# Performance work log

Measured on AMD Instinct MI355X. Metric: run time of the kernel, lower is better.

Reference implementation:

```python
import jax, jax.numpy as jnp
import numpy as np

EMBED_DIM = 1024
NUM_HEADS = 8
PROJ_DIM = EMBED_DIM // NUM_HEADS  # 128
SIGMA = 1.0        # attn_param
DISP = 1           # attn_displacement
BATCH = 8
SEQ_LEN = 2048
# per-head hard-coded attention positions (length == num_heads)
POSITIONS = ['center', 'left', 'right', 'first', 'last', 'center', 'left', 'right']


def _head_centers(L):
    """Center of the analytic Gaussian per head and per query position. [H, L]"""
    i = jnp.arange(L, dtype=jnp.float32)
    centers = []
    for pos in POSITIONS:
        if pos == 'center':
            c = i
        elif pos == 'left':
            c = i - DISP
        elif pos == 'right':
            c = i + DISP
        elif pos == 'first':
            c = jnp.zeros_like(i)
        else:  # 'last' (no padding: last valid index is L-1)
            c = jnp.full_like(i, L - 1)
        centers.append(c)
    return jnp.stack(centers)  # [H, L]


def setup_inputs() -> dict:
    key = jax.random.key(0)
    k1, k2, k3 = jax.random.split(key, 3)
    x = jax.random.normal(k1, (BATCH, SEQ_LEN, EMBED_DIM), dtype=jnp.float32)
    # xavier-ish scale for square weights
    s = (6.0 / (EMBED_DIM + EMBED_DIM)) ** 0.5
    W_in = jax.random.uniform(k2, (EMBED_DIM, EMBED_DIM), dtype=jnp.float32, minval=-s, maxval=s)
    W_out = jax.random.uniform(k3, (EMBED_DIM, EMBED_DIM), dtype=jnp.float32, minval=-s, maxval=s)
    return {"x": x, "W_in": W_in, "W_out": W_out}


def reference(x, W_in, W_out):
    B, L, E = x.shape
    H, P = NUM_HEADS, PROJ_DIM
    # value projection (F.linear with input_weights), split into heads
    v = (x @ W_in.T).reshape(B, L, H, P).transpose(0, 2, 1, 3)  # [B, H, L, P]
    # analytic per-head attention weights: Gaussian in key-position around center
    j = jnp.arange(L, dtype=jnp.float32)
    c = _head_centers(L)                                         # [H, Lq]
    logits = -((j[None, None, :] - c[:, :, None]) ** 2) / (2.0 * SIGMA ** 2)  # [H, Lq, Lk]
    w = jax.nn.softmax(logits, axis=-1)                          # [H, Lq, Lk]
    # weighted value aggregation (torch.bmm(attn_weights, values) per head)
    attended = jnp.einsum('hqk,bhkp->bhqp', w, v)                # [B, H, L, P]
    attended = attended.transpose(0, 2, 1, 3).reshape(B, L, E)
    # bias-free output projection
    return attended @ W_out.T
```

## Files before the change

### kernel.cpp

```cpp
#include <hip/hip_runtime.h>
#include <stdint.h>

typedef unsigned short u16;
typedef unsigned int   u32;

typedef float  f32x4  __attribute__((ext_vector_type(4)));
typedef __bf16 bf16x8 __attribute__((ext_vector_type(8)));

__device__ __forceinline__ u16 f2bf(float f) {
  union { float f; u32 u; } c; c.f = f;
  u32 u = c.u + 0x7fffu + ((c.u >> 16) & 1u);
  return (u16)(u >> 16);
}
__device__ __forceinline__ float bf2f(u16 h) {
  union { u32 u; float f; } c; c.u = ((u32)h) << 16;
  return c.f;
}
__device__ __forceinline__ void gll16(const void* g, void* l) {
  __builtin_amdgcn_global_load_lds(
      (const __attribute__((address_space(1))) void*)g,
      (__attribute__((address_space(3))) void*)l, 16, 0, 0);
}

__global__ __launch_bounds__(256)
void cvt_all(const float4* __restrict__ x,  uint2* __restrict__ xb,  int n4x,
             const float4* __restrict__ wi, uint2* __restrict__ wib,
             const float4* __restrict__ wo, uint2* __restrict__ wob, int n4w) {
  int i = blockIdx.x * 256 + threadIdx.x;
  const float4* s; uint2* d; int j;
  if (i < n4x)            { s = x;  d = xb;  j = i; }
  else if (i < n4x + n4w) { s = wi; d = wib; j = i - n4x; }
  else                    { s = wo; d = wob; j = i - n4x - n4w; }
  float4 v = s[j];
  uint2 o;
  o.x = (u32)f2bf(v.x) | ((u32)f2bf(v.y) << 16);
  o.y = (u32)f2bf(v.z) | ((u32)f2bf(v.w) << 16);
  d[j] = o;
}

template <bool OUT_BF16>
__global__ __launch_bounds__(512, 2)
void gemm_nt_256(const u16* __restrict__ A, const u16* __restrict__ B,
                 void* __restrict__ Cout, int M, int N, int K) {
  __shared__ u16 Ls[65536];
  const int tid  = threadIdx.x;
  const int lane = tid & 63;
  const int wave = tid >> 6;
  const int wm   = wave >> 2;
  const int wn   = wave & 3;
  const int ml   = lane & 15;
  const int q    = lane >> 4;
  const int qx   = q ^ (ml & 3);
  const int hx   = (ml >> 2) & 1;

  const int flat = blockIdx.y * 4 + blockIdx.x;
  const int xcd  = flat & 7;
  const int slot = flat >> 3;
  const int mt   = xcd * (gridDim.y >> 3) + (slot >> 2);
  const int nt   = slot & 3;
  const int m0   = mt * 256;
  const int n0   = nt * 256;

  const int srr = tid >> 3;
  const int gc  = (tid & 7) ^ ((tid >> 3) & 7);
  const u16* Agb = A + (size_t)(m0 + srr) * K + gc * 8;
  const u16* Bgb = B + (size_t)(n0 + srr) * K + gc * 8;
  char* LsB = (char*)Ls;
  const int wlds = wave * 1024;

  auto stageA = [&](int bufb, int h, int k0) {
    char* d = LsB + bufb + h * 16384 + wlds;
    gll16(Agb + (size_t)(h * 128) * K + k0, d);
    gll16(Agb + (size_t)(h * 128 + 64) * K + k0, d + 8192);
  };
  auto stageB = [&](int bufb, int h, int k0) {
    char* d = LsB + bufb + 32768 + h * 16384 + wlds;
    gll16(Bgb + (size_t)(h * 128) * K + k0, d);
    gll16(Bgb + (size_t)(h * 128 + 64) * K + k0, d + 8192);
  };

  const int aB_ = wm * 8192 + ml * 64 + qx * 8;
  const int bB_ = 16384 + (wn >> 1) * 8192 + ((wn & 1) * 64 + ml) * 64 + qx * 8;

  f32x4  acc[8][4] = {};
  bf16x8 fa0[4], fa1[4], B0[4], B1[4];

  auto rdA = [&](bf16x8* dst, int bw, int MH, int s) {
    const int so = (s ^ hx) * 32;
#pragma unroll
    for (int i = 0; i < 4; ++i)
      dst[i] = *reinterpret_cast<const bf16x8*>(&Ls[bw + aB_ + MH * 4096 + i * 1024 + so]);
  };
  auto rdB = [&](bf16x8* dst, int bw, int s) {
    const int so = (s ^ hx) * 32;
#pragma unroll
    for (int j = 0; j < 4; ++j)
      dst[j] = *reinterpret_cast<const bf16x8*>(&Ls[bw + bB_ + j * 1024 + so]);
  };
  auto mfma16 = [&](int mh, const bf16x8* a, const bf16x8* b) {
    __builtin_amdgcn_s_setprio(1);
#pragma unroll
    for (int i = 0; i < 4; ++i)
#pragma unroll
      for (int j = 0; j < 4; ++j)
        acc[mh * 4 + i][j] = __builtin_amdgcn_mfma_f32_16x16x32_bf16(
            a[i], b[j], acc[mh * 4 + i][j], 0, 0, 0);
    __builtin_amdgcn_s_setprio(0);
  };
  auto barrier = [&] {
    __builtin_amdgcn_sched_barrier(0);
    __builtin_amdgcn_s_barrier();
  };

  stageB(0, 0, 0);      stageB(0, 1, 0);
  stageA(0, 0, 0);      stageA(0, 1, 0);
  stageB(65536, 0, 64); stageB(65536, 1, 64);
  stageA(65536, 0, 64); stageA(65536, 1, 64);
  asm volatile("s_waitcnt vmcnt(8)" ::: "memory");
  barrier();
  rdA(fa0, 0, 0, 0);
  rdB(B0, 0, 0);

  const int NT = K >> 6;
  int bufb = 0;
  for (int t = 0; t < NT; ++t, bufb ^= 65536) {
    const int  bw     = bufb >> 1;
    const int  bwn    = (bufb ^ 65536) >> 1;
    const bool rdnext = (t + 1 < NT);
    const bool stg    = (t + 2 < NT);
    const int  kst    = (t + 2) << 6;
    mfma16(0, fa0, B0);
    rdA(fa1, bw, 0, 1); rdB(B1, bw, 1);
    barrier();
    mfma16(0, fa1, B1);
    rdA(fa0, bw, 1, 0);
    if (stg) { stageB(bufb, 0, kst); stageB(bufb, 1, kst); }
    barrier();
    mfma16(1, fa0, B0);
    rdA(fa1, bw, 1, 1);
    if (stg)         { asm volatile("s_waitcnt vmcnt(4)" ::: "memory"); }
    else if (rdnext) { asm volatile("s_waitcnt vmcnt(0)" ::: "memory"); }
    barrier();
    mfma16(1, fa1, B1);
    if (rdnext) { rdA(fa0, bwn, 0, 0); rdB(B0, bwn, 0); }
    if (stg) { stageA(bufb, 0, kst); stageA(bufb, 1, kst); }
    barrier();
  }

  const int rowb = m0 + wm * 128 + q * 4;
  const int colb = n0 + wn * 64 + ml;
#pragma unroll
  for (int mf = 0; mf < 8; ++mf)
#pragma unroll
    for (int nf = 0; nf < 4; ++nf)
#pragma unroll
      for (int r = 0; r < 4; ++r) {
        size_t idx = (size_t)(rowb + mf * 16 + r) * N + (colb + nf * 16);
        float val = acc[mf][nf][r];
        if (OUT_BF16) ((u16*)Cout)[idx] = f2bf(val);
        else          ((float*)Cout)[idx] = val;
      }
}

__global__ __launch_bounds__(256)
void gauss_conv(const u16* __restrict__ v, u16* __restrict__ att, int L) {
  constexpr float wt[13] = {
    1.5229979744712628e-08f, 3.7266531720786709e-06f, 3.3546262790251185e-04f,
    1.1108996538242306e-02f, 1.3533528323661270e-01f, 6.0653065971263342e-01f,
    1.0f,
    6.0653065971263342e-01f, 1.3533528323661270e-01f, 1.1108996538242306e-02f,
    3.3546262790251185e-04f, 3.7266531720786709e-06f, 1.5229979744712628e-08f
  };
  const int t  = threadIdx.x;
  const int fg = t & 15;
  const int li = t >> 4;
  const int l  = blockIdx.x * 16 + li;
  const int h  = blockIdx.y;
  const int b  = blockIdx.z;
  int c;
  switch (h) {
    case 0: case 5: c = l;     break;
    case 1: case 6: c = l - 1; break;
    case 2: case 7: c = l + 1; break;
    case 3:         c = 0;     break;
    default:        c = L - 1; break;
  }
  const int fbase = h * 128 + fg * 8;
  const u16* vb = v + (size_t)b * L * 1024 + fbase;

  float a[8] = {};
  float Z = 0.f;
#pragma unroll
  for (int d = -6; d <= 6; ++d) {
    int idx = c + d;
    bool ok = (idx >= 0) && (idx < L);
    int ic_ = idx < 0 ? 0 : (idx >= L ? L - 1 : idx);
    float w = ok ? wt[d + 6] : 0.f;
    Z += w;
    uint4 p = *reinterpret_cast<const uint4*>(vb + (size_t)ic_ * 1024);
    a[0] = fmaf(w, bf2f((u16)(p.x & 0xffffu)), a[0]);
    a[1] = fmaf(w, bf2f((u16)(p.x >> 16)),     a[1]);
    a[2] = fmaf(w, bf2f((u16)(p.y & 0xffffu)), a[2]);
    a[3] = fmaf(w, bf2f((u16)(p.y >> 16)),     a[3]);
    a[4] = fmaf(w, bf2f((u16)(p.z & 0xffffu)), a[4]);
    a[5] = fmaf(w, bf2f((u16)(p.z >> 16)),     a[5]);
    a[6] = fmaf(w, bf2f((u16)(p.w & 0xffffu)), a[6]);
    a[7] = fmaf(w, bf2f((u16)(p.w >> 16)),     a[7]);
  }
  float inv = 1.0f / Z;
  uint4 o;
  o.x = (u32)f2bf(a[0] * inv) | ((u32)f2bf(a[1] * inv) << 16);
  o.y = (u32)f2bf(a[2] * inv) | ((u32)f2bf(a[3] * inv) << 16);
  o.z = (u32)f2bf(a[4] * inv) | ((u32)f2bf(a[5] * inv) << 16);
  o.w = (u32)f2bf(a[6] * inv) | ((u32)f2bf(a[7] * inv) << 16);
  *reinterpret_cast<uint4*>(att + (size_t)(b * L + l) * 1024 + fbase) = o;
}

extern "C" void kernel_launch(void* const* d_in, const int* in_sizes, int n_in,
                              void* d_out, int out_size, void* d_ws, size_t ws_size,
                              hipStream_t stream) {
  const int Bb = 8, L = 2048, E = 1024;
  const int M = Bb * L, N = E, K = E;

  const float* x  = (const float*)d_in[0];
  const float* Wi = (const float*)d_in[1];
  const float* Wo = (const float*)d_in[2];
  float* out = (float*)d_out;

  size_t offV  = (size_t)M * E * 2;
  size_t offWi = offV + (size_t)M * E * 2;
  size_t offWo = offWi + (size_t)E * E * 2;
  size_t need  = offWo + (size_t)E * E * 2;
  if (ws_size < need) return;

  u16* xb  = (u16*)d_ws;
  u16* v   = (u16*)((char*)d_ws + offV);
  u16* wib = (u16*)((char*)d_ws + offWi);
  u16* wob = (u16*)((char*)d_ws + offWo);
  u16* att = xb;

  int n4x = M * E / 4, n4w = E * E / 4;
  int nblk = (n4x + 2 * n4w) / 256;
  cvt_all<<<nblk, 256, 0, stream>>>((const float4*)x, (uint2*)xb, n4x,
                                    (const float4*)Wi, (uint2*)wib,
                                    (const float4*)Wo, (uint2*)wob, n4w);

  dim3 gg(N / 256, M / 256);
  gemm_nt_256<true ><<<gg, 512, 0, stream>>>(xb,  wib, v,   M, N, K);
  gauss_conv<<<dim3(L / 16, 8, Bb), 256, 0, stream>>>(v, att, L);
  gemm_nt_256<false><<<gg, 512, 0, stream>>>(att, wob, out, M, N, K);
}
```

Measured before the change: 210.5 us.

## Restructure GEMM main loop into quadrant-based single-prefetch schedule

Result: no change. 213.7 us (+1.5%).

```diff
diff --git a/kernel.cpp b/kernel.cpp
--- a/kernel.cpp
+++ b/kernel.cpp
@@ -68,83 +68,84 @@
   char* LsB = (char*)Ls;
   const int wlds = wave * 1024;
 
-  auto stageA = [&](int bufb, int h, int k0) {
-    char* d = LsB + bufb + h * 16384 + wlds;
-    gll16(Agb + (size_t)(h * 128) * K + k0, d);
-    gll16(Agb + (size_t)(h * 128 + 64) * K + k0, d + 8192);
-  };
-  auto stageB = [&](int bufb, int h, int k0) {
-    char* d = LsB + bufb + 32768 + h * 16384 + wlds;
-    gll16(Bgb + (size_t)(h * 128) * K + k0, d);
-    gll16(Bgb + (size_t)(h * 128 + 64) * K + k0, d + 8192);
+  auto stageAll = [&](int bufb, int k0) {
+#pragma unroll
+    for (int h = 0; h < 2; ++h) {
+      char* d = LsB + bufb + h * 16384 + wlds;
+      gll16(Agb + (size_t)(h * 128) * K + k0, d);
+      gll16(Agb + (size_t)(h * 128 + 64) * K + k0, d + 8192);
+    }
+#pragma unroll
+    for (int h = 0; h < 2; ++h) {
+      char* d = LsB + bufb + 32768 + h * 16384 + wlds;
+      gll16(Bgb + (size_t)(h * 128) * K + k0, d);
+      gll16(Bgb + (size_t)(h * 128 + 64) * K + k0, d + 8192);
+    }
   };
 
   const int aB_ = wm * 8192 + ml * 64 + qx * 8;
   const int bB_ = 16384 + (wn >> 1) * 8192 + ((wn & 1) * 64 + ml) * 64 + qx * 8;
 
   f32x4  acc[8][4] = {};
-  bf16x8 fa0[4], fa1[4], B0[4], B1[4];
-
-  auto rdA = [&](bf16x8* dst, int bw, int MH, int s) {
-    const int so = (s ^ hx) * 32;
+  bf16x8 af[4][2];
+  bf16x8 bq[2][2][2];
+
+  auto rdA = [&](int bw, int mh) {
 #pragma unroll
     for (int i = 0; i < 4; ++i)
-      dst[i] = *reinterpret_cast<const bf16x8*>(&Ls[bw + aB_ + MH * 4096 + i * 1024 + so]);
-  };
-  auto rdB = [&](bf16x8* dst, int bw, int s) {
-    const int so = (s ^ hx) * 32;
-#pragma unroll
-    for (int j = 0; j < 4; ++j)
-      dst[j] = *reinterpret_cast<const bf16x8*>(&Ls[bw + bB_ + j * 1024 + so]);
-  };
-  auto mfma16 = [&](int mh, const bf16x8* a, const bf16x8* b) {
+#pragma unroll
+      for (int s = 0; s < 2; ++s)
+        af[i][s] = *reinterpret_cast<const bf16x8*>(
+            &Ls[bw + aB_ + mh * 4096 + i * 1024 + (s ^ hx) * 32]);
+  };
+  auto rdB = [&](int bw, int nh) {
+#pragma unroll
+    for (int j = 0; j < 2; ++j)
+#pragma unroll
+      for (int s = 0; s < 2; ++s)
+        bq[nh][j][s] = *reinterpret_cast<const bf16x8*>(
+            &Ls[bw + bB_ + nh * 2048 + j * 1024 + (s ^ hx) * 32]);
+  };
+  auto mfmaQ = [&](int mh, int nh) {
     __builtin_amdgcn_s_setprio(1);
 #pragma unroll
-    for (int i = 0; i < 4; ++i)
-#pragma unroll
-      for (int j = 0; j < 4; ++j)
-        acc[mh * 4 + i][j] = __builtin_amdgcn_mfma_f32_16x16x32_bf16(
-            a[i], b[j], acc[mh * 4 + i][j], 0, 0, 0);
+    for (int s = 0; s < 2; ++s)
+#pragma unroll
+      for (int i = 0; i < 4; ++i)
+#pragma unroll
+        for (int j = 0; j < 2; ++j)
+          acc[mh * 4 + i][nh * 2 + j] = __builtin_amdgcn_mfma_f32_16x16x32_bf16(
+              af[i][s], bq[nh][j][s], acc[mh * 4 + i][nh * 2 + j], 0, 0, 0);
     __builtin_amdgcn_s_setprio(0);
   };
-  auto barrier = [&] {
-    __builtin_amdgcn_sched_barrier(0);
-    __builtin_amdgcn_s_barrier();
-  };
-
-  stageB(0, 0, 0);      stageB(0, 1, 0);
-  stageA(0, 0, 0);      stageA(0, 1, 0);
-  stageB(65536, 0, 64); stageB(65536, 1, 64);
-  stageA(65536, 0, 64); stageA(65536, 1, 64);
-  asm volatile("s_waitcnt vmcnt(8)" ::: "memory");
-  barrier();
-  rdA(fa0, 0, 0, 0);
-  rdB(B0, 0, 0);
+
+  stageAll(0, 0);
+  asm volatile("s_waitcnt vmcnt(0)" ::: "memory");
+  __builtin_amdgcn_s_barrier();
 
   const int NT = K >> 6;
   int bufb = 0;
   for (int t = 0; t < NT; ++t, bufb ^= 65536) {
-    const int  bw     = bufb >> 1;
-    const int  bwn    = (bufb ^ 65536) >> 1;
-    const bool rdnext = (t + 1 < NT);
-    const bool stg    = (t + 2 < NT);
-    const int  kst    = (t + 2) << 6;
-    mfma16(0, fa0, B0);
-    rdA(fa1, bw, 0, 1); rdB(B1, bw, 1);
-    barrier();
-    mfma16(0, fa1, B1);
-    rdA(fa0, bw, 1, 0);
-    if (stg) { stageB(bufb, 0, kst); stageB(bufb, 1, kst); }
-    barrier();
-    mfma16(1, fa0, B0);
-    rdA(fa1, bw, 1, 1);
-    if (stg)         { asm volatile("s_waitcnt vmcnt(4)" ::: "memory"); }
-    else if (rdnext) { asm volatile("s_waitcnt vmcnt(0)" ::: "memory"); }
-    barrier();
-    mfma16(1, fa1, B1);
-    if (rdnext) { rdA(fa0, bwn, 0, 0); rdB(B0, bwn, 0); }
-    if (stg) { stageA(bufb, 0, kst); stageA(bufb, 1, kst); }
-    barrier();
+    const int bw = bufb >> 1;
+    rdA(bw, 0); rdB(bw, 0);
+    if (t + 1 < NT) stageAll(bufb ^ 65536, (t + 1) << 6);
+    __builtin_amdgcn_s_barrier();
+    asm volatile("s_waitcnt lgkmcnt(0)" ::: "memory");
+    mfmaQ(0, 0);
+    __builtin_amdgcn_s_barrier();
+    rdB(bw, 1);
+    __builtin_amdgcn_s_barrier();
+    asm volatile("s_waitcnt lgkmcnt(0)" ::: "memory");
+    mfmaQ(0, 1);
+    __builtin_amdgcn_s_barrier();
+    rdA(bw, 1);
+    __builtin_amdgcn_s_barrier();
+    asm volatile("s_waitcnt lgkmcnt(0)" ::: "memory");
+    mfmaQ(1, 1);
+    __builtin_amdgcn_s_barrier();
+    mfmaQ(1, 0);
+    asm volatile("s_waitcnt vmcnt(0)" ::: "memory");
+    __builtin_amdgcn_s_barrier();
   }
 
   const int rowb = m0 + wm * 128 + q * 4;
```
